# Kernel tuning notes

Measured on AMD Instinct MI355X. Metric: run time of the kernel, lower is better.

## Reference

```python
import jax, jax.numpy as jnp
import numpy as np

HEADS = 8
DIM_HEAD = 64
SCALE = DIM_HEAD ** -0.5
POS_DIM = 64


def _sincos_pe(H, W, dim, dtype):
    # matches build_2d_sincos_pos_embed: [1, dim, H, W]
    y = jnp.linspace(-1.0, 1.0, H)[:, None] * jnp.ones((1, W), jnp.float32)
    x = jnp.ones((H, 1), jnp.float32) * jnp.linspace(-1.0, 1.0, W)[None, :]
    omega = 1.0 / (10000.0 ** (jnp.arange(dim // 4, dtype=jnp.float32) / (dim // 4)))
    px = x[..., None] * omega  # [H, W, dim//4]
    py = y[..., None] * omega
    pe = jnp.concatenate([jnp.sin(px), jnp.cos(px), jnp.sin(py), jnp.cos(py)], axis=-1)
    return pe.transpose(2, 0, 1)[None].astype(dtype)


def _conv2d(x, w):
    return jax.lax.conv_general_dilated(
        x, w, (1, 1), 'SAME', dimension_numbers=('NCHW', 'OIHW', 'NCHW'))


def _sobel(d):
    kx = jnp.array([[1, 0, -1], [2, 0, -2], [1, 0, -1]], jnp.float32).reshape(1, 1, 3, 3)
    ky = jnp.array([[1, 2, 1], [0, 0, 0], [-1, -2, -1]], jnp.float32).reshape(1, 1, 3, 3)
    return _conv2d(d, kx), _conv2d(d, ky)


def setup_inputs() -> dict:
    key = jax.random.key(0)
    ks = jax.random.split(key, 8)
    B, C, H, W = 2, 256, 64, 64
    hid = HEADS * DIM_HEAD  # 512
    s = 0.02
    return {
        'x': jax.random.normal(ks[0], (B, C, H, W), jnp.float32),
        'dsm': jax.random.uniform(ks[1], (B, 1, H, W), jnp.float32),
        'wq': jax.random.normal(ks[2], (hid, C), jnp.float32) * s,
        'wkv': jax.random.normal(ks[3], (2 * hid, C + 1), jnp.float32) * s,
        'wout': jax.random.normal(ks[4], (C, hid), jnp.float32) * s,
        'bout': jnp.zeros((C,), jnp.float32),
        'w_hape': jax.random.normal(ks[5], (hid, POS_DIM + 3), jnp.float32) * s,
        'b_hape': jnp.zeros((hid,), jnp.float32),
        'w_alpha': jax.random.normal(ks[6], (1, 1, 3, 3), jnp.float32) * 0.1,
        'b_alpha': jnp.zeros((1,), jnp.float32),
    }


def reference(x, dsm, wq, wkv, wout, bout, w_hape, b_hape, w_alpha, b_alpha):
    B, C, H, W = x.shape
    hid = wq.shape[0]
    # per-sample min-max normalize DSM over spatial dims
    dmin = dsm.min(axis=(2, 3), keepdims=True)
    dmax = dsm.max(axis=(2, 3), keepdims=True)
    d = (dsm - dmin) / (dmax - dmin + 1e-6)
    # HAPE: [PE | h | grad_h] -> 1x1 conv to hidden
    pe = jnp.broadcast_to(_sincos_pe(H, W, POS_DIM, x.dtype), (B, POS_DIM, H, W))
    gx, gy = _sobel(d)
    hape_in = jnp.concatenate([pe, d, gx, gy], axis=1)  # [B, 67, H, W]
    hape_k = jnp.einsum('oc,bchw->bohw', w_hape, hape_in) + b_hape[None, :, None, None]
    # QKV via 1x1 convs
    q = jnp.einsum('oc,bchw->bohw', wq, x)
    kv = jnp.einsum('oc,bchw->bohw', wkv, jnp.concatenate([x, d], axis=1))
    k = kv[:, :hid] + hape_k
    v = kv[:, hid:]
    to_heads = lambda t: t.reshape(B, HEADS, DIM_HEAD, H * W)  # b (h c) x y -> b h c (xy)
    qh = to_heads(q) * SCALE
    kh = to_heads(k)
    vh = to_heads(v)
    sim = jnp.einsum('bhdi,bhdj->bhij', qh, kh)  # [B, h, N, N]
    attn = jax.nn.softmax(sim, axis=-1)
    out = jnp.einsum('bhij,bhdj->bhid', attn, vh)  # [B, h, N, d]
    # b h (x y) d -> b (h d) x y
    out = out.transpose(0, 1, 3, 2).reshape(B, HEADS * DIM_HEAD, H, W)
    out = jnp.einsum('oc,bchw->bohw', wout, out) + bout[None, :, None, None]
    # fine: gradient-magnitude alpha gating
    mag = jnp.sqrt(jnp.maximum(gx, 0.0) ** 2 + jnp.maximum(gy, 0.0) ** 2 + 1e-12)
    alpha = jax.nn.sigmoid(_conv2d(mag, w_alpha) + b_alpha[None, :, None, None])
    return x + out * alpha
```

## Files before the change

kernel.cpp:

```cpp
#include <hip/hip_runtime.h>
#include <math.h>

#define NPOS 4096
#define MTOT 8192
#define KP   352
#define HT 64
#define WT 64
#define NSPLIT 2
#define KEYS_PER (NPOS / NSPLIT)
#define NCH (KEYS_PER / 64)

typedef unsigned short ushortT;
typedef short v8s __attribute__((ext_vector_type(8)));
typedef float v4f __attribute__((ext_vector_type(4)));
typedef unsigned uint2v __attribute__((ext_vector_type(2)));

static __device__ __forceinline__ ushortT bfr(float f) {
    union { float f; unsigned u; } v; v.f = f;
    return (ushortT)((v.u + 0x8000u) >> 16);
}
static __device__ __forceinline__ unsigned pack2bf(float a, float b) {
    union { float f; unsigned u; } ua, ub; ua.f = a; ub.f = b;
    return __builtin_amdgcn_perm(ub.u + 0x8000u, ua.u + 0x8000u, 0x07060302u);
}
static __device__ __forceinline__ unsigned pack2bf_t(float a, float b) {
    union { float f; unsigned u; } ua, ub; ua.f = a; ub.f = b;
    return __builtin_amdgcn_perm(ub.u, ua.u, 0x07060302u);
}
static __device__ __forceinline__ float fexp2(float x) {
#if __has_builtin(__builtin_amdgcn_exp2f)
    return __builtin_amdgcn_exp2f(x);
#else
    return exp2f(x);
#endif
}

__global__ void k_prep(const float* __restrict__ dsm,
                       const float* __restrict__ walpha, const float* __restrict__ balpha,
                       ushortT* __restrict__ F, float* __restrict__ alpha) {
    int idx = blockIdx.x * 256 + threadIdx.x;
    int b = idx / NPOS, n = idx % NPOS;
    int hh = n / WT, ww = n % WT;
    const float* dp = dsm + (size_t)b * NPOS;

    float mn = 1e30f, mx = -1e30f;
    for (int i = threadIdx.x; i < NPOS; i += 256) {
        float v = dp[i];
        mn = fminf(mn, v); mx = fmaxf(mx, v);
    }
    for (int off = 32; off; off >>= 1) {
        mn = fminf(mn, __shfl_xor(mn, off, 64));
        mx = fmaxf(mx, __shfl_xor(mx, off, 64));
    }
    __shared__ float smn[4], smx[4];
    int wid = threadIdx.x >> 6;
    if ((threadIdx.x & 63) == 0) { smn[wid] = mn; smx[wid] = mx; }
    __syncthreads();
    float dmin = fminf(fminf(smn[0], smn[1]), fminf(smn[2], smn[3]));
    float dmax = fmaxf(fmaxf(smx[0], smx[1]), fmaxf(smx[2], smx[3]));
    float inv = 1.0f / (dmax - dmin + 1e-6f);

    float dwin[5][5];
    #pragma unroll
    for (int dy = 0; dy < 5; dy++)
        #pragma unroll
        for (int dx = 0; dx < 5; dx++) {
            int y = hh + dy - 2, x = ww + dx - 2;
            float v = 0.0f;
            if (y >= 0 && y < HT && x >= 0 && x < WT) v = (dp[y * WT + x] - dmin) * inv;
            dwin[dy][dx] = v;
        }

    float gxc = 0.f, gyc = 0.f;
    float conv = 0.f;
    #pragma unroll
    for (int oy = 0; oy < 3; oy++)
        #pragma unroll
        for (int ox = 0; ox < 3; ox++) {
            int qy = hh + oy - 1, qx = ww + ox - 1;
            float m = 0.0f;
            if (qy >= 0 && qy < HT && qx >= 0 && qx < WT) {
                float gx = dwin[oy][ox] - dwin[oy][ox + 2]
                         + 2.f * dwin[oy + 1][ox] - 2.f * dwin[oy + 1][ox + 2]
                         + dwin[oy + 2][ox] - dwin[oy + 2][ox + 2];
                float gy = dwin[oy][ox] + 2.f * dwin[oy][ox + 1] + dwin[oy][ox + 2]
                         - dwin[oy + 2][ox] - 2.f * dwin[oy + 2][ox + 1] - dwin[oy + 2][ox + 2];
                if (oy == 1 && ox == 1) { gxc = gx; gyc = gy; }
                float rx = fmaxf(gx, 0.f), ry = fmaxf(gy, 0.f);
                m = sqrtf(rx * rx + ry * ry + 1e-12f);
            }
            conv += walpha[oy * 3 + ox] * m;
        }
    alpha[idx] = 1.f / (1.f + __expf(-(conv + balpha[0])));

    ushortT* fb = F + (size_t)idx * KP;
    fb[256] = bfr(dwin[2][2]);
    fb[257] = bfr(gxc);
    fb[258] = bfr(gyc);
    float xc = -1.f + 2.f * (float)ww / 63.f;
    float yc = -1.f + 2.f * (float)hh / 63.f;
    const float l2w = 13.287712379549449f;
    #pragma unroll
    for (int i = 0; i < 16; i++) {
        float omega = exp2f(-(float)i * (l2w / 16.f));
        float px = xc * omega, py = yc * omega;
        fb[259 + i]      = bfr(__sinf(px));
        fb[259 + 16 + i] = bfr(__cosf(px));
        fb[259 + 32 + i] = bfr(__sinf(py));
        fb[259 + 48 + i] = bfr(__cosf(py));
    }
    #pragma unroll
    for (int z = 323; z < KP; z++) fb[z] = 0;
}

__global__ void k_cast(const float* __restrict__ x, ushortT* __restrict__ F) {
    __shared__ __align__(16) ushortT Tl[64][72];
    int nt = blockIdx.x * 64;
    int b = blockIdx.y >> 2, ct = (blockIdx.y & 3) * 64;
    int t = threadIdx.x;
    #pragma unroll
    for (int rep = 0; rep < 4; rep++) {
        int row = rep * 16 + (t >> 4), c4 = (t & 15) * 4;
        float4 f4 = *(const float4*)&x[((size_t)(b * 256 + ct + row)) * NPOS + nt + c4];
        Tl[c4 + 0][row] = bfr(f4.x);
        Tl[c4 + 1][row] = bfr(f4.y);
        Tl[c4 + 2][row] = bfr(f4.z);
        Tl[c4 + 3][row] = bfr(f4.w);
    }
    __syncthreads();
    #pragma unroll
    for (int rep = 0; rep < 2; rep++) {
        int slot = rep * 256 + t, row = slot >> 3, c8 = slot & 7;
        *(uint4*)&F[((size_t)(b * 4096 + nt + row)) * KP + ct + c8 * 8] = *(uint4*)&Tl[row][c8 * 8];
    }
}

__global__ void k_wcprep(const float* __restrict__ wq, const float* __restrict__ wkv,
                         const float* __restrict__ whape, const float* __restrict__ bhape,
                         const float* __restrict__ wout,
                         ushortT* __restrict__ Wc, float* __restrict__ biasc,
                         ushortT* __restrict__ woutb) {
    int idx = blockIdx.x * 256 + threadIdx.x;
    if (blockIdx.x < 512) {
        woutb[idx] = bfr(wout[idx]);
    }
    int o = idx / KP, k = idx % KP;
    float v = 0.f;
    if (o < 512) {
        if (k < 256) v = wq[o * 256 + k] * 0.18033688011112042f;
        if (k == 0) biasc[o] = 0.f;
    } else if (o < 1024) {
        int r = o - 512;
        if (k < 257) v = wkv[r * 257 + k];
        if (k == 256)      v += whape[r * 67 + 64];
        else if (k == 257) v = whape[r * 67 + 65];
        else if (k == 258) v = whape[r * 67 + 66];
        else if (k >= 259 && k < 323) v = whape[r * 67 + (k - 259)];
        if (k == 0) biasc[o] = bhape[r];
    } else {
        int r = o - 512;
        if (k < 257) v = wkv[r * 257 + k];
        if (k == 0) biasc[o] = 0.f;
    }
    Wc[idx] = bfr(v);
}

__global__ __launch_bounds__(256) void k_gemm1(const ushortT* __restrict__ Wc, const ushortT* __restrict__ F,
                                               const float* __restrict__ biasc,
                                               ushortT* __restrict__ qT, ushortT* __restrict__ kT,
                                               ushortT* __restrict__ vv) {
    __shared__ __align__(16) ushortT Al[128][40];
    __shared__ __align__(16) ushortT Bl[64][40];
    __shared__ __align__(16) ushortT Vt[128][72];
    int mt = blockIdx.x * 64;
    int ot = blockIdx.y * 128;
    int t = threadIdx.x, w = t >> 6, lane = t & 63, u = lane & 15, quad = lane >> 4;
    int ar0 = t >> 2, ac0 = t & 3;
    int ar1 = 64 + ar0;
    int br = t >> 2, bc = t & 3;
    v4f acc[2][4] = {};
    for (int k0 = 0; k0 < KP; k0 += 32) {
        __syncthreads();
        *(uint4*)&Al[ar0][ac0 * 8] = *(const uint4*)&Wc[(size_t)(ot + ar0) * KP + k0 + ac0 * 8];
        *(uint4*)&Al[ar1][ac0 * 8] = *(const uint4*)&Wc[(size_t)(ot + ar1) * KP + k0 + ac0 * 8];
        *(uint4*)&Bl[br][bc * 8]   = *(const uint4*)&F[(size_t)(mt + br) * KP + k0 + bc * 8];
        __syncthreads();
        v8s a0 = *(v8s*)&Al[w * 32 + u][quad * 8];
        v8s a1 = *(v8s*)&Al[w * 32 + 16 + u][quad * 8];
        #pragma unroll
        for (int n4 = 0; n4 < 4; n4++) {
            v8s bb = *(v8s*)&Bl[n4 * 16 + u][quad * 8];
            acc[0][n4] = __builtin_amdgcn_mfma_f32_16x16x32_bf16(a0, bb, acc[0][n4], 0, 0, 0);
            acc[1][n4] = __builtin_amdgcn_mfma_f32_16x16x32_bf16(a1, bb, acc[1][n4], 0, 0, 0);
        }
    }
    float bo[2][4];
    #pragma unroll
    for (int rr = 0; rr < 2; rr++)
        #pragma unroll
        for (int r = 0; r < 4; r++) bo[rr][r] = biasc[ot + w * 32 + rr * 16 + quad * 4 + r];
    if (ot < 1024) {
        ushortT* dst = (ot < 512) ? qT : kT;
        #pragma unroll
        for (int rr = 0; rr < 2; rr++) {
            int oo = ot + w * 32 + rr * 16;
            int h = (oo >> 6) & 7;
            int dcol = (oo & 63) + quad * 4;
            #pragma unroll
            for (int n4 = 0; n4 < 4; n4++) {
                int m = mt + n4 * 16 + u;
                uint2 val;
                val.x = pack2bf(acc[rr][n4][0] + bo[rr][0], acc[rr][n4][1] + bo[rr][1]);
                val.y = pack2bf(acc[rr][n4][2] + bo[rr][2], acc[rr][n4][3] + bo[rr][3]);
                *(uint2*)&dst[((size_t)h * MTOT + m) * 64 + dcol] = val;
            }
        }
    } else {
        __syncthreads();
        #pragma unroll
        for (int rr = 0; rr < 2; rr++)
            #pragma unroll
            for (int n4 = 0; n4 < 4; n4++) {
                int ml = n4 * 16 + u;
                #pragma unroll
                for (int r = 0; r < 4; r++)
                    Vt[w * 32 + rr * 16 + quad * 4 + r][ml] = bfr(acc[rr][n4][r] + bo[rr][r]);
            }
        __syncthreads();
        #pragma unroll
        for (int rep = 0; rep < 4; rep++) {
            int slot = rep * 256 + t, row = slot >> 3, c8 = slot & 7;
            *(uint4*)&vv[(size_t)(ot - 1024 + row) * MTOT + mt + c8 * 8] = *(uint4*)&Vt[row][c8 * 8];
        }
    }
}

#define LIDX(row, cb) (((row) << 6) + ((((cb) ^ ((row) & 7))) << 3))
__global__ __launch_bounds__(256, 4) void k_flash(const ushortT* __restrict__ qT,
                                                  const ushortT* __restrict__ kT,
                                                  const ushortT* __restrict__ vv,
                                                  float* __restrict__ Opart,
                                                  float* __restrict__ liPart) {
    __shared__ __align__(16) ushortT Kbuf[2][64 * 64];
    __shared__ __align__(16) ushortT Vbuf[2][64 * 64];

    int it = blockIdx.x;
    int bh = blockIdx.y;
    int half = blockIdx.z;
    int b = bh >> 3, h = bh & 7;
    int colbase = b * NPOS;
    int t = threadIdx.x, w = t >> 6, lane = t & 63, u = lane & 15, quad = lane >> 4;
    int qb = it * 128 + w * 32;

    const ushortT* Qg = qT + ((size_t)h * MTOT + colbase + qb) * 64;
    const ushortT* Kg = kT + ((size_t)h * MTOT + colbase + half * KEYS_PER) * 64;
    const ushortT* Vg = vv + ((size_t)(h * 64)) * MTOT + colbase + half * KEYS_PER;

    int row0 = t >> 3, c80 = t & 7;
    int row1 = 32 + row0;

    v8s bq[2][2];
    #pragma unroll
    for (int g = 0; g < 2; g++)
        #pragma unroll
        for (int hf = 0; hf < 2; hf++)
            bq[g][hf] = *(const v8s*)&Qg[(size_t)(g * 16 + u) * 64 + hf * 32 + quad * 8];

    v8s ones;
    #pragma unroll
    for (int i = 0; i < 8; i++) ones[i] = (short)0x3F80;

    v4f li4[2] = {};
    v4f O[4][2] = {};

    uint4 kr0 = *(const uint4*)&Kg[(size_t)row0 * 64 + c80 * 8];
    uint4 kr1 = *(const uint4*)&Kg[(size_t)row1 * 64 + c80 * 8];
    uint4 vr0 = *(const uint4*)&Vg[(size_t)row0 * MTOT + c80 * 8];
    uint4 vr1 = *(const uint4*)&Vg[(size_t)row1 * MTOT + c80 * 8];

    #pragma unroll 2
    for (int jc = 0; jc < NCH; jc++) {
        int cur = jc & 1;
        *(uint4*)&Kbuf[cur][LIDX(row0, c80)] = kr0;
        *(uint4*)&Kbuf[cur][LIDX(row1, c80)] = kr1;
        *(uint4*)&Vbuf[cur][LIDX(row0, c80)] = vr0;
        *(uint4*)&Vbuf[cur][LIDX(row1, c80)] = vr1;
        __syncthreads();
        if (jc + 1 < NCH) {
            int jb = (jc + 1) * 64;
            kr0 = *(const uint4*)&Kg[(size_t)(jb + row0) * 64 + c80 * 8];
            kr1 = *(const uint4*)&Kg[(size_t)(jb + row1) * 64 + c80 * 8];
            vr0 = *(const uint4*)&Vg[(size_t)row0 * MTOT + jb + c80 * 8];
            vr1 = *(const uint4*)&Vg[(size_t)row1 * MTOT + jb + c80 * 8];
        }

        const ushortT* Kb = &Kbuf[cur][0];
        const ushortT* Vb = &Vbuf[cur][0];

        v8s bp[2][2];
        #pragma unroll
        for (int kp = 0; kp < 2; kp++) {
            unsigned pk0[2][2], pk1[2][2];
            #pragma unroll
            for (int kk = 0; kk < 2; kk++) {
                int k4 = kp * 2 + kk;
                v8s ak0 = *(const v8s*)&Kb[LIDX(k4 * 16 + u, quad)];
                v8s ak1 = *(const v8s*)&Kb[LIDX(k4 * 16 + u, 4 + quad)];
                v4f st[2];
                #pragma unroll
                for (int g = 0; g < 2; g++) {
                    st[g] = (v4f){0.f, 0.f, 0.f, 0.f};
                    st[g] = __builtin_amdgcn_mfma_f32_16x16x32_bf16(ak0, bq[g][0], st[g], 0, 0, 0);
                    st[g] = __builtin_amdgcn_mfma_f32_16x16x32_bf16(ak1, bq[g][1], st[g], 0, 0, 0);
                }
                #pragma unroll
                for (int g = 0; g < 2; g++) {
                    float p0 = fexp2(st[g][0]);
                    float p1 = fexp2(st[g][1]);
                    float p2 = fexp2(st[g][2]);
                    float p3 = fexp2(st[g][3]);
                    pk0[g][kk] = pack2bf_t(p0, p1);
                    pk1[g][kk] = pack2bf_t(p2, p3);
                }
            }
            #pragma unroll
            for (int g = 0; g < 2; g++) {
                uint2v r0s = __builtin_amdgcn_permlane32_swap(pk0[g][0], pk0[g][1], false, false);
                uint2v r1s = __builtin_amdgcn_permlane32_swap(pk1[g][0], pk1[g][1], false, false);
                uint2v t0 = __builtin_amdgcn_permlane16_swap(r0s.x, r0s.y, false, false);
                uint2v t1 = __builtin_amdgcn_permlane16_swap(r1s.x, r1s.y, false, false);
                union { uint4 u4; v8s s; } cv;
                cv.u4.x = t0.x; cv.u4.y = t1.x; cv.u4.z = t0.y; cv.u4.w = t1.y;
                bp[g][kp] = cv.s;
            }
        }

        #pragma unroll
        for (int g = 0; g < 2; g++) {
            li4[g] = __builtin_amdgcn_mfma_f32_16x16x32_bf16(ones, bp[g][0], li4[g], 0, 0, 0);
            li4[g] = __builtin_amdgcn_mfma_f32_16x16x32_bf16(ones, bp[g][1], li4[g], 0, 0, 0);
        }

        #pragma unroll
        for (int d4 = 0; d4 < 4; d4++) {
            v8s av0 = *(const v8s*)&Vb[LIDX(d4 * 16 + u, quad)];
            v8s av1 = *(const v8s*)&Vb[LIDX(d4 * 16 + u, 4 + quad)];
            #pragma unroll
            for (int g = 0; g < 2; g++) {
                O[d4][g] = __builtin_amdgcn_mfma_f32_16x16x32_bf16(av0, bp[g][0], O[d4][g], 0, 0, 0);
                O[d4][g] = __builtin_amdgcn_mfma_f32_16x16x32_bf16(av1, bp[g][1], O[d4][g], 0, 0, 0);
            }
        }
    }

    #pragma unroll
    for (int g = 0; g < 2; g++) {
        int q = qb + g * 16 + u;
        size_t m2 = (size_t)(half * 2 + b) * 4096 + q;
        size_t base = m2 * 512 + h * 64;
        #pragma unroll
        for (int d4 = 0; d4 < 4; d4++) {
            float4 o4;
            o4.x = O[d4][g][0]; o4.y = O[d4][g][1]; o4.z = O[d4][g][2]; o4.w = O[d4][g][3];
            *(float4*)&Opart[base + d4 * 16 + quad * 4] = o4;
        }
        if (quad == 0) liPart[m2 * 8 + h] = li4[g][0];
    }
}

__global__ __launch_bounds__(256) void k_comb(const float* __restrict__ Opart,
                                              const float* __restrict__ liPart,
                                              ushortT* __restrict__ aoB) {
    int tid = blockIdx.x * 256 + threadIdx.x;
    int m = tid >> 7, c4 = (tid & 127) * 4, h = c4 >> 6;
    float l = 0.f;
    #pragma unroll
    for (int s = 0; s < NSPLIT; s++) l += liPart[((size_t)s * 8192 + m) * 8 + h];
    float inv = 1.f / l;
    float ox = 0.f, oy = 0.f, oz = 0.f, ow = 0.f;
    #pragma unroll
    for (int s = 0; s < NSPLIT; s++) {
        float4 o = *(const float4*)&Opart[((size_t)s * 8192 + m) * 512 + c4];
        ox += o.x; oy += o.y; oz += o.z; ow += o.w;
    }
    uint2 val;
    val.x = pack2bf(ox * inv, oy * inv);
    val.y = pack2bf(oz * inv, ow * inv);
    *(uint2*)&aoB[(size_t)m * 512 + c4] = val;
}

__global__ __launch_bounds__(256) void k_gemm2(const ushortT* __restrict__ woutb, const ushortT* __restrict__ aoB,
                                               const float* __restrict__ bout, const float* __restrict__ x,
                                               const float* __restrict__ alpha, float* __restrict__ out) {
    __shared__ __align__(16) ushortT Al[64][40];
    __shared__ __align__(16) ushortT Bl[64][40];
    int mt = blockIdx.x * 64;
    int ot = blockIdx.y * 64;
    int t = threadIdx.x, w = t >> 6, lane = t & 63, u = lane & 15, quad = lane >> 4;
    int arow = t >> 2, ac8 = t & 3;
    v4f acc[4] = {};
    for (int k0 = 0; k0 < 512; k0 += 32) {
        __syncthreads();
        *(uint4*)&Al[arow][ac8 * 8] = *(const uint4*)&woutb[(size_t)(ot + arow) * 512 + k0 + ac8 * 8];
        *(uint4*)&Bl[arow][ac8 * 8] = *(const uint4*)&aoB[(size_t)(mt + arow) * 512 + k0 + ac8 * 8];
        __syncthreads();
        v8s a = *(v8s*)&Al[w * 16 + u][quad * 8];
        #pragma unroll
        for (int n4 = 0; n4 < 4; n4++) {
            v8s bb = *(v8s*)&Bl[n4 * 16 + u][quad * 8];
            acc[n4] = __builtin_amdgcn_mfma_f32_16x16x32_bf16(a, bb, acc[n4], 0, 0, 0);
        }
    }
    int b = mt >> 12, n0 = mt & 4095;
    int obase = ot + w * 16 + quad * 4;
    float bo[4];
    #pragma unroll
    for (int r = 0; r < 4; r++) bo[r] = bout[obase + r];
    #pragma unroll
    for (int n4 = 0; n4 < 4; n4++) {
        int n = n0 + n4 * 16 + u;
        float al = alpha[(size_t)b * NPOS + n];
        #pragma unroll
        for (int r = 0; r < 4; r++) {
            size_t xi = ((size_t)(b * 256 + obase + r)) * NPOS + n;
            out[xi] = x[xi] + (acc[n4][r] + bo[r]) * al;
        }
    }
}

extern "C" void kernel_launch(void* const* d_in, const int* in_sizes, int n_in,
                              void* d_out, int out_size, void* d_ws, size_t ws_size,
                              hipStream_t stream) {
    const float* x      = (const float*)d_in[0];
    const float* dsm    = (const float*)d_in[1];
    const float* wq     = (const float*)d_in[2];
    const float* wkv    = (const float*)d_in[3];
    const float* wout   = (const float*)d_in[4];
    const float* bout   = (const float*)d_in[5];
    const float* whape  = (const float*)d_in[6];
    const float* bhape  = (const float*)d_in[7];
    const float* walpha = (const float*)d_in[8];
    const float* balpha = (const float*)d_in[9];
    float* out = (float*)d_out;
    float* ws  = (float*)d_ws;

    size_t off = 0;
    float* alpha = ws + off; off += (size_t)2 * NPOS;
    float* biasc = ws + off; off += 2048;
    float* Opart  = ws + off; off += (size_t)NSPLIT * MTOT * 512;
    float* liPart = ws + off; off += (size_t)NSPLIT * MTOT * 8;
    ushortT* F     = (ushortT*)(ws + off); off += (size_t)MTOT * KP / 2;
    ushortT* Wc    = (ushortT*)(ws + off); off += (size_t)1536 * KP / 2;
    ushortT* woutb = (ushortT*)(ws + off); off += (size_t)256 * 512 / 2;
    ushortT* qT    = (ushortT*)(ws + off); off += (size_t)8 * MTOT * 64 / 2;
    ushortT* kT    = (ushortT*)(ws + off); off += (size_t)8 * MTOT * 64 / 2;
    ushortT* vv    = (ushortT*)(ws + off); off += (size_t)512 * MTOT / 2;
    ushortT* aoB   = (ushortT*)(ws + off); off += (size_t)MTOT * 512 / 2;
    (void)in_sizes; (void)n_in; (void)out_size; (void)ws_size;

    k_prep<<<32, 256, 0, stream>>>(dsm, walpha, balpha, F, alpha);
    k_cast<<<dim3(64, 8), 256, 0, stream>>>(x, F);
    k_wcprep<<<(1536 * KP) / 256, 256, 0, stream>>>(wq, wkv, whape, bhape, wout, Wc, biasc, woutb);
    k_gemm1<<<dim3(128, 12), 256, 0, stream>>>(Wc, F, biasc, qT, kT, vv);
    k_flash<<<dim3(32, 16, NSPLIT), 256, 0, stream>>>(qT, kT, vv, Opart, liPart);
    k_comb<<<4096, 256, 0, stream>>>(Opart, liPart, aoB);
    k_gemm2<<<dim3(128, 4), 256, 0, stream>>>(woutb, aoB, bout, x, alpha, out);
}
```

Measured before the change: 202.6 us.

## Precompute LDS offsets, add MFMA priority hints, and tabulate positional encoding

```diff
diff --git a/kernel.cpp b/kernel.cpp
--- a/kernel.cpp
+++ b/kernel.cpp
@@ -38,10 +38,27 @@
 __global__ void k_prep(const float* __restrict__ dsm,
                        const float* __restrict__ walpha, const float* __restrict__ balpha,
                        ushortT* __restrict__ F, float* __restrict__ alpha) {
+    __shared__ ushortT tab[64][32];
+    __shared__ float smn[4], smx[4];
+
     int idx = blockIdx.x * 256 + threadIdx.x;
     int b = idx / NPOS, n = idx % NPOS;
     int hh = n / WT, ww = n % WT;
     const float* dp = dsm + (size_t)b * NPOS;
+    const float l2w = 13.287712379549449f;
+
+    {
+        int t = threadIdx.x;
+        #pragma unroll
+        for (int e8 = 0; e8 < 8; e8++) {
+            int e = t * 8 + e8;
+            int c = e >> 5, j = e & 31, i = j & 15;
+            float coord = -1.f + 2.f * (float)c / 63.f;
+            float omega = exp2f(-(float)i * (l2w / 16.f));
+            float v = (j < 16) ? __sinf(coord * omega) : __cosf(coord * omega);
+            tab[c][j] = bfr(v);
+        }
+    }
 
     float mn = 1e30f, mx = -1e30f;
     for (int i = threadIdx.x; i < NPOS; i += 256) {
@@ -52,7 +69,6 @@
         mn = fminf(mn, __shfl_xor(mn, off, 64));
         mx = fmaxf(mx, __shfl_xor(mx, off, 64));
     }
-    __shared__ float smn[4], smx[4];
     int wid = threadIdx.x >> 6;
     if ((threadIdx.x & 63) == 0) { smn[wid] = mn; smx[wid] = mx; }
     __syncthreads();
@@ -97,18 +113,10 @@
     fb[256] = bfr(dwin[2][2]);
     fb[257] = bfr(gxc);
     fb[258] = bfr(gyc);
-    float xc = -1.f + 2.f * (float)ww / 63.f;
-    float yc = -1.f + 2.f * (float)hh / 63.f;
-    const float l2w = 13.287712379549449f;
-    #pragma unroll
-    for (int i = 0; i < 16; i++) {
-        float omega = exp2f(-(float)i * (l2w / 16.f));
-        float px = xc * omega, py = yc * omega;
-        fb[259 + i]      = bfr(__sinf(px));
-        fb[259 + 16 + i] = bfr(__cosf(px));
-        fb[259 + 32 + i] = bfr(__sinf(py));
-        fb[259 + 48 + i] = bfr(__cosf(py));
-    }
+    #pragma unroll
+    for (int i = 0; i < 32; i++) fb[259 + i] = tab[ww][i];
+    #pragma unroll
+    for (int i = 0; i < 32; i++) fb[291 + i] = tab[hh][i];
     #pragma unroll
     for (int z = 323; z < KP; z++) fb[z] = 0;
 }
@@ -259,6 +267,17 @@
     int row0 = t >> 3, c80 = t & 7;
     int row1 = 32 + row0;
 
+    unsigned boff[4][2];
+    #pragma unroll
+    for (int i4 = 0; i4 < 4; i4++) {
+        boff[i4][0] = 2u * (unsigned)LIDX(i4 * 16 + u, quad);
+        boff[i4][1] = 2u * (unsigned)LIDX(i4 * 16 + u, 4 + quad);
+        asm volatile("" : "+v"(boff[i4][0]), "+v"(boff[i4][1]));
+    }
+    unsigned woff0 = 2u * (unsigned)LIDX(row0, c80);
+    unsigned woff1 = 2u * (unsigned)LIDX(row1, c80);
+    asm volatile("" : "+v"(woff0), "+v"(woff1));
+
     v8s bq[2][2];
     #pragma unroll
     for (int g = 0; g < 2; g++)
@@ -281,10 +300,12 @@
     #pragma unroll 2
     for (int jc = 0; jc < NCH; jc++) {
         int cur = jc & 1;
-        *(uint4*)&Kbuf[cur][LIDX(row0, c80)] = kr0;
-        *(uint4*)&Kbuf[cur][LIDX(row1, c80)] = kr1;
-        *(uint4*)&Vbuf[cur][LIDX(row0, c80)] = vr0;
-        *(uint4*)&Vbuf[cur][LIDX(row1, c80)] = vr1;
+        char* KbW = (char*)&Kbuf[cur][0];
+        char* VbW = (char*)&Vbuf[cur][0];
+        *(uint4*)(KbW + woff0) = kr0;
+        *(uint4*)(KbW + woff1) = kr1;
+        *(uint4*)(VbW + woff0) = vr0;
+        *(uint4*)(VbW + woff1) = vr1;
         __syncthreads();
         if (jc + 1 < NCH) {
             int jb = (jc + 1) * 64;
@@ -294,8 +315,8 @@
             vr1 = *(const uint4*)&Vg[(size_t)row1 * MTOT + jb + c80 * 8];
         }
 
-        const ushortT* Kb = &Kbuf[cur][0];
-        const ushortT* Vb = &Vbuf[cur][0];
+        const char* Kb = (const char*)&Kbuf[cur][0];
+        const char* Vb = (const char*)&Vbuf[cur][0];
 
         v8s bp[2][2];
         #pragma unroll
@@ -304,15 +325,17 @@
             #pragma unroll
             for (int kk = 0; kk < 2; kk++) {
                 int k4 = kp * 2 + kk;
-                v8s ak0 = *(const v8s*)&Kb[LIDX(k4 * 16 + u, quad)];
-                v8s ak1 = *(const v8s*)&Kb[LIDX(k4 * 16 + u, 4 + quad)];
+                v8s ak0 = *(const v8s*)(Kb + boff[k4][0]);
+                v8s ak1 = *(const v8s*)(Kb + boff[k4][1]);
                 v4f st[2];
+                __builtin_amdgcn_s_setprio(1);
                 #pragma unroll
                 for (int g = 0; g < 2; g++) {
                     st[g] = (v4f){0.f, 0.f, 0.f, 0.f};
                     st[g] = __builtin_amdgcn_mfma_f32_16x16x32_bf16(ak0, bq[g][0], st[g], 0, 0, 0);
                     st[g] = __builtin_amdgcn_mfma_f32_16x16x32_bf16(ak1, bq[g][1], st[g], 0, 0, 0);
                 }
+                __builtin_amdgcn_s_setprio(0);
                 #pragma unroll
                 for (int g = 0; g < 2; g++) {
                     float p0 = fexp2(st[g][0]);
@@ -335,22 +358,23 @@
             }
         }
 
+        __builtin_amdgcn_s_setprio(1);
         #pragma unroll
         for (int g = 0; g < 2; g++) {
             li4[g] = __builtin_amdgcn_mfma_f32_16x16x32_bf16(ones, bp[g][0], li4[g], 0, 0, 0);
             li4[g] = __builtin_amdgcn_mfma_f32_16x16x32_bf16(ones, bp[g][1], li4[g], 0, 0, 0);
         }
-
         #pragma unroll
         for (int d4 = 0; d4 < 4; d4++) {
-            v8s av0 = *(const v8s*)&Vb[LIDX(d4 * 16 + u, quad)];
-            v8s av1 = *(const v8s*)&Vb[LIDX(d4 * 16 + u, 4 + quad)];
+            v8s av0 = *(const v8s*)(Vb + boff[d4][0]);
+            v8s av1 = *(const v8s*)(Vb + boff[d4][1]);
             #pragma unroll
             for (int g = 0; g < 2; g++) {
                 O[d4][g] = __builtin_amdgcn_mfma_f32_16x16x32_bf16(av0, bp[g][0], O[d4][g], 0, 0, 0);
                 O[d4][g] = __builtin_amdgcn_mfma_f32_16x16x32_bf16(av1, bp[g][1], O[d4][g], 0, 0, 0);
             }
         }
+        __builtin_amdgcn_s_setprio(0);
     }
 
     #pragma unroll
```

Measured after the change: 205.2 us. No clear change (+1.3%).
